# Kernel optimization log

Hardware: AMD Instinct MI355X
Metric: run time of the kernel (lower is better)

Reference implementation:

```python
import jax, jax.numpy as jnp
import numpy as np

N_NODES = 100000
N_USERS = 60000
N_MOVIES = 40000
N_EDGES = 1200000
D_IN = 64
D_EMB = 64


def setup_inputs() -> dict:
    key = jax.random.key(0)
    ks = jax.random.split(key, 6)
    x = jax.random.normal(ks[0], (N_NODES, D_IN), dtype=jnp.float32)
    edge_index = jax.random.randint(ks[1], (2, N_EDGES), 0, N_NODES, dtype=jnp.int64)
    # Glorot-ish init for the two GCNConv linear weights
    W1 = jax.random.normal(ks[2], (D_IN, D_EMB), dtype=jnp.float32) * (1.0 / np.sqrt(D_IN))
    b1 = jnp.zeros((D_EMB,), dtype=jnp.float32)
    W2 = jax.random.normal(ks[3], (D_EMB, D_EMB), dtype=jnp.float32) * (1.0 / np.sqrt(D_EMB))
    b2 = jnp.zeros((D_EMB,), dtype=jnp.float32)
    return {"x": x, "edge_index": edge_index, "W1": W1, "b1": b1, "W2": W2, "b2": b2}


def gcn_conv(x, W, b, src, dst):
    """PyG GCNConv: D^{-1/2}(A+I)D^{-1/2} X W + b with symmetric norm and self-loops."""
    h = x @ W  # [N, D_out]
    ones = jnp.ones(src.shape[0], dtype=h.dtype)
    # degree includes self-loop (+1)
    deg = jax.ops.segment_sum(ones, dst, num_segments=N_NODES) + 1.0
    dinv = jax.lax.rsqrt(deg)  # [N]
    coef = dinv[src] * dinv[dst]  # [E]
    agg = jax.ops.segment_sum(h[src] * coef[:, None], dst, num_segments=N_NODES)
    # self-loop contribution: norm = dinv[i]^2
    return agg + h * (dinv * dinv)[:, None] + b


def reference(x, edge_index, W1, b1, W2, b2):
    src, dst = edge_index[0], edge_index[1]
    h = gcn_conv(x, W1, b1, src, dst)
    h = jax.nn.relu(h)  # dropout is identity in eval mode
    h = gcn_conv(h, W2, b2, src, dst)
    user = h[:N_USERS]
    movie = h[N_USERS:N_USERS + N_MOVIES]
    return user, movie, h
```

## Files before the change

### kernel.cpp

```cpp
#include <hip/hip_runtime.h>

#define NN 100000
#define NE 1200000
#define DD 64
#define NPART 8
#define PSZ (NN / NPART)
#define EPB 4096
#define NCHUNK ((NE + EPB - 1) / EPB)
#define SCH 1024
#define SNB ((NN + SCH - 1) / SCH)

#define KCH3 96
#define CEH3 (NE / KCH3)
#define P3 2
#define BINS3 (NN / P3)
#define BINW3 (BINS3 / 4)
#define KSEG 4
#define KPS (KCH3 / KSEG)
#define NW4 (NN / 4)

static __device__ __forceinline__ unsigned short f2bf(float f) {
    unsigned int u = __float_as_uint(f);
    u += 0x7fffu + ((u >> 16) & 1u);
    return (unsigned short)(u >> 16);
}
static __device__ __forceinline__ float bf_lo(unsigned int u) {
    return __uint_as_float(u << 16);
}
static __device__ __forceinline__ float bf_hi(unsigned int u) {
    return __uint_as_float(u & 0xffff0000u);
}

__global__ __launch_bounds__(1024) void k_hist3(const int* __restrict__ dst,
                                                unsigned char* __restrict__ H,
                                                unsigned char* __restrict__ rank8) {
    __shared__ unsigned int bins[BINW3];
    int k = blockIdx.x >> 1;
    int p = blockIdx.x & 1;
    int t = threadIdx.x;
    for (int i = t; i < BINW3; i += 1024) bins[i] = 0u;
    __syncthreads();
    int lo = p * BINS3;
    int beg = k * CEH3;
    for (int e4 = beg + t * 4; e4 < beg + CEH3; e4 += 4096) {
        int4 d4 = *(const int4*)&dst[e4];
        int dd[4] = {d4.x, d4.y, d4.z, d4.w};
#pragma unroll
        for (int j = 0; j < 4; ++j) {
            unsigned int r = (unsigned int)(dd[j] - lo);
            if (r < (unsigned int)BINS3) {
                unsigned int sh = (r & 3u) << 3;
                unsigned int old = atomicAdd(&bins[r >> 2], 1u << sh);
                rank8[e4 + j] = (unsigned char)((old >> sh) & 0xffu);
            }
        }
    }
    __syncthreads();
    unsigned int* Hw = (unsigned int*)(H + (size_t)k * NN + lo);
    for (int i = t; i < BINW3; i += 1024) Hw[i] = bins[i];
}

__global__ __launch_bounds__(256) void k_cseg_sum(const unsigned int* __restrict__ H32,
                                                  unsigned int* __restrict__ aux) {
    int wd = blockIdx.x * 256 + threadIdx.x;
    int seg = blockIdx.y;
    if (wd >= NW4) return;
    unsigned int s = 0;
#pragma unroll
    for (int k = 0; k < KPS; ++k)
        s += H32[(size_t)(seg * KPS + k) * NW4 + wd];
    aux[seg * NW4 + wd] = s;
}

__global__ __launch_bounds__(256) void k_cseg_scan(unsigned int* __restrict__ H32,
                                                   const unsigned int* __restrict__ aux,
                                                   int* __restrict__ degi) {
    int wd = blockIdx.x * 256 + threadIdx.x;
    int seg = blockIdx.y;
    if (wd >= NW4) return;
    unsigned int base = 0;
    for (int i = 0; i < seg; ++i) base += aux[i * NW4 + wd];
    unsigned int s = base;
#pragma unroll
    for (int k = 0; k < KPS; ++k) {
        size_t idx = (size_t)(seg * KPS + k) * NW4 + wd;
        unsigned int v = H32[idx];
        H32[idx] = s;
        s += v;
    }
    if (seg == KSEG - 1) {
        int4 dg;
        dg.x = (int)(s & 0xffu);
        dg.y = (int)((s >> 8) & 0xffu);
        dg.z = (int)((s >> 16) & 0xffu);
        dg.w = (int)(s >> 24);
        *(int4*)&degi[4 * wd] = dg;
    }
}

__global__ __launch_bounds__(256) void k_fill3(const int* __restrict__ src,
                                               const int* __restrict__ dst,
                                               const unsigned char* __restrict__ rank8,
                                               const unsigned char* __restrict__ H,
                                               const int* __restrict__ rowptr,
                                               int* __restrict__ csr) {
    int e4 = (blockIdx.x * 256 + threadIdx.x) * 4;
    if (e4 >= NE) return;
    int4 d4 = *(const int4*)&dst[e4];
    int4 s4 = *(const int4*)&src[e4];
    unsigned int r4 = *(const unsigned int*)&rank8[e4];
    int dd[4] = {d4.x, d4.y, d4.z, d4.w};
    int ss[4] = {s4.x, s4.y, s4.z, s4.w};
    int k = e4 / CEH3;
#pragma unroll
    for (int j = 0; j < 4; ++j) {
        int d = dd[j];
        int base = rowptr[d] + (int)H[(size_t)k * NN + d];
        csr[base + (int)((r4 >> (8 * j)) & 0xffu)] = ss[j];
    }
}

__global__ void k_hist_rank(const int* __restrict__ dst, int* __restrict__ degi,
                            int* __restrict__ rank, int ne) {
    int i = blockIdx.x * blockDim.x + threadIdx.x;
    if (i < ne) rank[i] = atomicAdd(&degi[dst[i]], 1);
}

__global__ __launch_bounds__(256) void k_hist(const int* __restrict__ dst,
                                              int* __restrict__ degi, int ne) {
    int part = blockIdx.x & (NPART - 1);
    int lo = part * PSZ, hi = lo + PSZ;
    int beg = (blockIdx.x >> 3) * EPB;
    int end = min(beg + EPB, ne);
    for (int e = beg + (int)threadIdx.x; e < end; e += 256) {
        int d = dst[e];
        if (d >= lo && d < hi) atomicAdd(&degi[d], 1);
    }
}

__global__ __launch_bounds__(256) void k_scan_local(const int* __restrict__ degi,
                                                    int* __restrict__ rowptr,
                                                    int* __restrict__ part,
                                                    float* __restrict__ dinv) {
    __shared__ int wsum[4];
    int t = threadIdx.x;
    int idx = blockIdx.x * SCH + t * 4;
    int d0 = 0, d1 = 0, d2 = 0, d3 = 0;
    if (idx + 3 < NN) {
        int4 v = *(const int4*)&degi[idx];
        d0 = v.x; d1 = v.y; d2 = v.z; d3 = v.w;
        float4 dv;
        dv.x = rsqrtf((float)d0 + 1.0f);
        dv.y = rsqrtf((float)d1 + 1.0f);
        dv.z = rsqrtf((float)d2 + 1.0f);
        dv.w = rsqrtf((float)d3 + 1.0f);
        *(float4*)&dinv[idx] = dv;
    } else {
        if (idx     < NN) { d0 = degi[idx];     dinv[idx]     = rsqrtf((float)d0 + 1.0f); }
        if (idx + 1 < NN) { d1 = degi[idx + 1]; dinv[idx + 1] = rsqrtf((float)d1 + 1.0f); }
        if (idx + 2 < NN) { d2 = degi[idx + 2]; dinv[idx + 2] = rsqrtf((float)d2 + 1.0f); }
        if (idx + 3 < NN) { d3 = degi[idx + 3]; dinv[idx + 3] = rsqrtf((float)d3 + 1.0f); }
    }
    int s = d0 + d1 + d2 + d3;
    int lane = t & 63;
    int incl = s;
#pragma unroll
    for (int off = 1; off < 64; off <<= 1) {
        int v = __shfl_up(incl, off);
        if (lane >= off) incl += v;
    }
    int wv = t >> 6;
    if (lane == 63) wsum[wv] = incl;
    __syncthreads();
    int woff = 0;
#pragma unroll
    for (int i = 0; i < 4; ++i) if (i < wv) woff += wsum[i];
    int excl = woff + incl - s;
    if (idx     < NN) rowptr[idx]     = excl;
    if (idx + 1 < NN) rowptr[idx + 1] = excl + d0;
    if (idx + 2 < NN) rowptr[idx + 2] = excl + d0 + d1;
    if (idx + 3 < NN) rowptr[idx + 3] = excl + d0 + d1 + d2;
    if (t == 255) part[blockIdx.x] = woff + incl;
}

__global__ __launch_bounds__(128) void k_scan_part(int* __restrict__ part) {
    __shared__ int sm[128];
    int t = threadIdx.x;
    int v = (t < SNB) ? part[t] : 0;
    sm[t] = v;
    __syncthreads();
    for (int off = 1; off < 128; off <<= 1) {
        int add = (t >= off) ? sm[t - off] : 0;
        __syncthreads();
        sm[t] += add;
        __syncthreads();
    }
    if (t < SNB) part[t] = sm[t] - v;
}

__global__ void k_scan_add(int* __restrict__ rowptr, const int* __restrict__ part) {
    int i = blockIdx.x * blockDim.x + threadIdx.x;
    if (i < NN) rowptr[i] += part[i >> 10];
    if (i == 0) rowptr[NN] = NE;
}

__global__ void k_fill_rank(const int* __restrict__ src, const int* __restrict__ dst,
                            const int* __restrict__ rank, const int* __restrict__ rowptr,
                            int* __restrict__ csr_src, int ne) {
    int e = blockIdx.x * blockDim.x + threadIdx.x;
    if (e < ne) csr_src[rowptr[dst[e]] + rank[e]] = src[e];
}

__global__ __launch_bounds__(256) void k_fill(const int* __restrict__ src,
                                              const int* __restrict__ dst,
                                              const int* __restrict__ rowptr,
                                              int* __restrict__ cnt,
                                              int* __restrict__ csr_src, int ne) {
    int part = blockIdx.x & (NPART - 1);
    int lo = part * PSZ, hi = lo + PSZ;
    int beg = (blockIdx.x >> 3) * EPB;
    int end = min(beg + EPB, ne);
    for (int e = beg + (int)threadIdx.x; e < end; e += 256) {
        int d = dst[e];
        if (d >= lo && d < hi) {
            int pos = rowptr[d] + atomicAdd(&cnt[d], 1);
            csr_src[pos] = src[e];
        }
    }
}

__global__ __launch_bounds__(256) void k_gemm_bf(const float* __restrict__ X,
                                                 const float* __restrict__ W,
                                                 unsigned short* __restrict__ Hb,
                                                 int nrows) {
    __shared__ float4 Ws4[64][16];
    __shared__ float  Xs[64][68];
    int tid = threadIdx.x;
    const float4* W4 = (const float4*)W;
    for (int i = tid; i < 64 * 16; i += 256) Ws4[i >> 4][i & 15] = W4[i];
    int row0 = blockIdx.x * 64;
    const float4* X4 = (const float4*)X;
    for (int i = tid; i < 64 * 16; i += 256) {
        int r = i >> 4, q = i & 15;
        int row = row0 + r;
        float4 v = make_float4(0.f, 0.f, 0.f, 0.f);
        if (row < nrows) v = X4[row * 16 + q];
        *((float4*)&Xs[r][q * 4]) = v;
    }
    __syncthreads();
    int c4 = tid & 15;
    int rg = tid >> 4;
    float4 acc0 = make_float4(0.f, 0.f, 0.f, 0.f);
    float4 acc1 = acc0, acc2 = acc0, acc3 = acc0;
#pragma unroll 4
    for (int k = 0; k < 64; ++k) {
        float4 w = Ws4[k][c4];
        float x0 = Xs[rg * 4 + 0][k];
        float x1 = Xs[rg * 4 + 1][k];
        float x2 = Xs[rg * 4 + 2][k];
        float x3 = Xs[rg * 4 + 3][k];
        acc0.x += x0 * w.x; acc0.y += x0 * w.y; acc0.z += x0 * w.z; acc0.w += x0 * w.w;
        acc1.x += x1 * w.x; acc1.y += x1 * w.y; acc1.z += x1 * w.z; acc1.w += x1 * w.w;
        acc2.x += x2 * w.x; acc2.y += x2 * w.y; acc2.z += x2 * w.z; acc2.w += x2 * w.w;
        acc3.x += x3 * w.x; acc3.y += x3 * w.y; acc3.z += x3 * w.z; acc3.w += x3 * w.w;
    }
    float4 accs[4] = {acc0, acc1, acc2, acc3};
#pragma unroll
    for (int i = 0; i < 4; ++i) {
        int row = row0 + rg * 4 + i;
        if (row < nrows) {
            ushort4 o;
            o.x = f2bf(accs[i].x); o.y = f2bf(accs[i].y);
            o.z = f2bf(accs[i].z); o.w = f2bf(accs[i].w);
            *((ushort4*)&Hb[row * 64 + c4 * 4]) = o;
        }
    }
}

__global__ __launch_bounds__(256) void k_reduce(const unsigned short* __restrict__ Hb,
                                                const int* __restrict__ rowptr,
                                                const int* __restrict__ csr_src,
                                                const float* __restrict__ dinv,
                                                const float* __restrict__ b,
                                                float* __restrict__ out0,
                                                float* __restrict__ out1,
                                                int do_relu) {
    int n = blockIdx.x * 4 + (threadIdx.x >> 6);
    if (n >= NN) return;
    int lane = threadIdx.x & 63;
    int eg = lane >> 3;
    int cg = lane & 7;
    float din = dinv[n];
    uint4 us = *(const uint4*)(Hb + (size_t)n * 64 + cg * 8);
    float acc[8];
#pragma unroll
    for (int j = 0; j < 8; ++j) acc[j] = 0.f;

    int e = rowptr[n], end = rowptr[n + 1];
    int idx0 = e + eg;
    bool v0 = idx0 < end;
    int s0 = v0 ? csr_src[idx0] : 0;
    float cf0 = v0 ? dinv[s0] * din : 0.f;
    uint4 u0 = *(const uint4*)(Hb + (size_t)s0 * 64 + cg * 8);
    int idx1 = e + 8 + eg;
    bool v1 = idx1 < end;
    int s1 = v1 ? csr_src[idx1] : 0;
    float cf1 = v1 ? dinv[s1] * din : 0.f;

#pragma unroll 2
    while (e < end) {
        uint4 u1 = *(const uint4*)(Hb + (size_t)s1 * 64 + cg * 8);
        int idx2 = e + 16 + eg;
        bool v2 = idx2 < end;
        int s2 = v2 ? csr_src[idx2] : 0;
        float cf2 = v2 ? dinv[s2] * din : 0.f;
        acc[0] += bf_lo(u0.x) * cf0;  acc[1] += bf_hi(u0.x) * cf0;
        acc[2] += bf_lo(u0.y) * cf0;  acc[3] += bf_hi(u0.y) * cf0;
        acc[4] += bf_lo(u0.z) * cf0;  acc[5] += bf_hi(u0.z) * cf0;
        acc[6] += bf_lo(u0.w) * cf0;  acc[7] += bf_hi(u0.w) * cf0;
        u0 = u1; cf0 = cf1;
        s1 = s2; cf1 = cf2;
        e += 8;
    }

#pragma unroll
    for (int j = 0; j < 8; ++j) {
        acc[j] += __shfl_xor(acc[j], 8);
        acc[j] += __shfl_xor(acc[j], 16);
        acc[j] += __shfl_xor(acc[j], 32);
    }

    if (lane < 8) {
        float dd = din * din;
        float4 b0 = *(const float4*)(b + cg * 8);
        float4 b1 = *(const float4*)(b + cg * 8 + 4);
        float4 o0, o1;
        o0.x = acc[0] + bf_lo(us.x) * dd + b0.x;
        o0.y = acc[1] + bf_hi(us.x) * dd + b0.y;
        o0.z = acc[2] + bf_lo(us.y) * dd + b0.z;
        o0.w = acc[3] + bf_hi(us.y) * dd + b0.w;
        o1.x = acc[4] + bf_lo(us.z) * dd + b1.x;
        o1.y = acc[5] + bf_hi(us.z) * dd + b1.y;
        o1.z = acc[6] + bf_lo(us.w) * dd + b1.z;
        o1.w = acc[7] + bf_hi(us.w) * dd + b1.w;
        if (do_relu) {
            o0.x = fmaxf(o0.x, 0.f); o0.y = fmaxf(o0.y, 0.f);
            o0.z = fmaxf(o0.z, 0.f); o0.w = fmaxf(o0.w, 0.f);
            o1.x = fmaxf(o1.x, 0.f); o1.y = fmaxf(o1.y, 0.f);
            o1.z = fmaxf(o1.z, 0.f); o1.w = fmaxf(o1.w, 0.f);
        }
        *(float4*)(out0 + (size_t)n * 64 + cg * 8)     = o0;
        *(float4*)(out0 + (size_t)n * 64 + cg * 8 + 4) = o1;
        if (out1) {
            *(float4*)(out1 + (size_t)n * 64 + cg * 8)     = o0;
            *(float4*)(out1 + (size_t)n * 64 + cg * 8 + 4) = o1;
        }
    }
}

__global__ void k_copy4(const float4* __restrict__ in, float4* __restrict__ out, int n4) {
    int i = blockIdx.x * blockDim.x + threadIdx.x;
    if (i < n4) out[i] = in[i];
}

extern "C" void kernel_launch(void* const* d_in, const int* in_sizes, int n_in,
                              void* d_out, int out_size, void* d_ws, size_t ws_size,
                              hipStream_t stream) {
    const float* x  = (const float*)d_in[0];
    const int*   ei = (const int*)d_in[1];
    const float* W1 = (const float*)d_in[2];
    const float* b1 = (const float*)d_in[3];
    const float* W2 = (const float*)d_in[4];
    const float* b2 = (const float*)d_in[5];
    const int* src = ei;
    const int* dst = ei + NE;

    float* A = (float*)d_out;
    float* B = (float*)d_out + (size_t)NN * DD;

    char* w = (char*)d_ws;
    size_t off = 0;
    auto alloc = [&](size_t bytes) { void* p = w + off; off += (bytes + 255) & ~(size_t)255; return p; };
    float* dinv   = (float*)alloc(NN * sizeof(float));
    int*   degi   = (int*)  alloc(NN * sizeof(int));
    int*   cnt    = (int*)  alloc(NN * sizeof(int));
    int*   rowptr = (int*)  alloc((NN + 1) * sizeof(int));
    int*   part   = (int*)  alloc(512 * sizeof(int));
    int*   csr    = (int*)  alloc(NE * sizeof(int));
    size_t off_common = off;
    void* uni = alloc((size_t)NN * DD * sizeof(unsigned short));
    size_t off_uni = off;
    size_t need_rank = off_common + (((size_t)NE * sizeof(int) + 255) & ~(size_t)255);

    bool new_path  = (ws_size >= off_uni);
    bool rank_path = !new_path && (ws_size >= need_rank);

    unsigned char* Hh    = (unsigned char*)uni;
    unsigned char* rank8 = (unsigned char*)uni + (size_t)KCH3 * NN;
    int*           rank  = (int*)uni;
    unsigned short* Bb   = new_path ? (unsigned short*)uni : (unsigned short*)B;
    bool bb_in_ws = new_path;

    if (new_path) {
        k_hist3<<<KCH3 * P3, 1024, 0, stream>>>(dst, Hh, rank8);
        dim3 cgrid((NW4 + 255) / 256, KSEG);
        k_cseg_sum<<<cgrid, 256, 0, stream>>>((unsigned int*)Hh, (unsigned int*)cnt);
        k_cseg_scan<<<cgrid, 256, 0, stream>>>((unsigned int*)Hh, (const unsigned int*)cnt, degi);
        k_scan_local<<<SNB, 256, 0, stream>>>(degi, rowptr, part, dinv);
        k_scan_part<<<1, 128, 0, stream>>>(part);
        k_scan_add<<<(NN + 255) / 256, 256, 0, stream>>>(rowptr, part);
        k_fill3<<<(NE / 4 + 255) / 256, 256, 0, stream>>>(src, dst, rank8, Hh, rowptr, csr);
    } else if (rank_path) {
        hipMemsetAsync(degi, 0, NN * sizeof(int), stream);
        k_hist_rank<<<(NE + 255) / 256, 256, 0, stream>>>(dst, degi, rank, NE);
        k_scan_local<<<SNB, 256, 0, stream>>>(degi, rowptr, part, dinv);
        k_scan_part<<<1, 128, 0, stream>>>(part);
        k_scan_add<<<(NN + 255) / 256, 256, 0, stream>>>(rowptr, part);
        k_fill_rank<<<(NE + 255) / 256, 256, 0, stream>>>(src, dst, rank, rowptr, csr, NE);
    } else {
        hipMemsetAsync(degi, 0, NN * sizeof(int), stream);
        hipMemsetAsync(cnt, 0, NN * sizeof(int), stream);
        k_hist<<<NCHUNK * NPART, 256, 0, stream>>>(dst, degi, NE);
        k_scan_local<<<SNB, 256, 0, stream>>>(degi, rowptr, part, dinv);
        k_scan_part<<<1, 128, 0, stream>>>(part);
        k_scan_add<<<(NN + 255) / 256, 256, 0, stream>>>(rowptr, part);
        k_fill<<<NCHUNK * NPART, 256, 0, stream>>>(src, dst, rowptr, cnt, csr, NE);
    }

    k_gemm_bf<<<(NN + 63) / 64, 256, 0, stream>>>(x, W1, Bb, NN);
    k_reduce<<<(NN + 3) / 4, 256, 0, stream>>>(Bb, rowptr, csr, dinv, b1, A, nullptr, 1);

    k_gemm_bf<<<(NN + 63) / 64, 256, 0, stream>>>(A, W2, Bb, NN);
    if (bb_in_ws) {
        k_reduce<<<(NN + 3) / 4, 256, 0, stream>>>(Bb, rowptr, csr, dinv, b2, A, B, 0);
    } else {
        k_reduce<<<(NN + 3) / 4, 256, 0, stream>>>(Bb, rowptr, csr, dinv, b2, A, nullptr, 0);
        k_copy4<<<(NN * DD / 4 + 255) / 256, 256, 0, stream>>>((const float4*)A, (float4*)B, NN * DD / 4);
    }
}
```

Before: 263.4 us.

## Assign one node per 8 lanes in reduce and split histogram into four partitions

The aggregation kernel now maps each node to 8 lanes, each owning 8 feature columns and walking the node's edges sequentially. Previously 64 lanes split the edges 8 ways and combined partial sums with cross-lane shuffles. This removes the shuffle reduction and the idle lanes in the epilogue, and packs 32 nodes per block instead of 4. In exchange each wavefront loops to the maximum degree among its 8 nodes, so degree imbalance costs extra iterations and per-lane latency chains get longer. Separately, the histogram kernel's partition count goes from 2 to 4, shrinking its shared-memory bin array and doubling its block count, which may raise occupancy.

```diff
diff --git a/kernel.cpp b/kernel.cpp
--- a/kernel.cpp
+++ b/kernel.cpp
@@ -12,7 +12,7 @@
 
 #define KCH3 96
 #define CEH3 (NE / KCH3)
-#define P3 2
+#define P3 4
 #define BINS3 (NN / P3)
 #define BINW3 (BINS3 / 4)
 #define KSEG 4
@@ -35,8 +35,8 @@
                                                 unsigned char* __restrict__ H,
                                                 unsigned char* __restrict__ rank8) {
     __shared__ unsigned int bins[BINW3];
-    int k = blockIdx.x >> 1;
-    int p = blockIdx.x & 1;
+    int k = blockIdx.x >> 2;
+    int p = blockIdx.x & 3;
     int t = threadIdx.x;
     for (int i = t; i < BINW3; i += 1024) bins[i] = 0u;
     __syncthreads();
@@ -285,34 +285,35 @@
                                                 float* __restrict__ out0,
                                                 float* __restrict__ out1,
                                                 int do_relu) {
-    int n = blockIdx.x * 4 + (threadIdx.x >> 6);
+    int n = blockIdx.x * 32 + (threadIdx.x >> 3);
     if (n >= NN) return;
-    int lane = threadIdx.x & 63;
-    int eg = lane >> 3;
-    int cg = lane & 7;
+    int cg = threadIdx.x & 7;
     float din = dinv[n];
     uint4 us = *(const uint4*)(Hb + (size_t)n * 64 + cg * 8);
+
+    int e0 = rowptr[n];
+    int deg = rowptr[n + 1] - e0;
+    int dmax = deg;
+    dmax = max(dmax, __shfl_xor(dmax, 8));
+    dmax = max(dmax, __shfl_xor(dmax, 16));
+    dmax = max(dmax, __shfl_xor(dmax, 32));
+
     float acc[8];
 #pragma unroll
     for (int j = 0; j < 8; ++j) acc[j] = 0.f;
 
-    int e = rowptr[n], end = rowptr[n + 1];
-    int idx0 = e + eg;
-    bool v0 = idx0 < end;
-    int s0 = v0 ? csr_src[idx0] : 0;
+    bool v0 = 0 < deg;
+    int s0 = v0 ? csr_src[e0] : 0;
     float cf0 = v0 ? dinv[s0] * din : 0.f;
     uint4 u0 = *(const uint4*)(Hb + (size_t)s0 * 64 + cg * 8);
-    int idx1 = e + 8 + eg;
-    bool v1 = idx1 < end;
-    int s1 = v1 ? csr_src[idx1] : 0;
+    bool v1 = 1 < deg;
+    int s1 = v1 ? csr_src[e0 + 1] : 0;
     float cf1 = v1 ? dinv[s1] * din : 0.f;
 
-#pragma unroll 2
-    while (e < end) {
+    for (int t = 0; t < dmax; ++t) {
         uint4 u1 = *(const uint4*)(Hb + (size_t)s1 * 64 + cg * 8);
-        int idx2 = e + 16 + eg;
-        bool v2 = idx2 < end;
-        int s2 = v2 ? csr_src[idx2] : 0;
+        bool v2 = (t + 2) < deg;
+        int s2 = v2 ? csr_src[e0 + t + 2] : 0;
         float cf2 = v2 ? dinv[s2] * din : 0.f;
         acc[0] += bf_lo(u0.x) * cf0;  acc[1] += bf_hi(u0.x) * cf0;
         acc[2] += bf_lo(u0.y) * cf0;  acc[3] += bf_hi(u0.y) * cf0;
@@ -320,41 +321,31 @@
         acc[6] += bf_lo(u0.w) * cf0;  acc[7] += bf_hi(u0.w) * cf0;
         u0 = u1; cf0 = cf1;
         s1 = s2; cf1 = cf2;
-        e += 8;
-    }
-
-#pragma unroll
-    for (int j = 0; j < 8; ++j) {
-        acc[j] += __shfl_xor(acc[j], 8);
-        acc[j] += __shfl_xor(acc[j], 16);
-        acc[j] += __shfl_xor(acc[j], 32);
-    }
-
-    if (lane < 8) {
-        float dd = din * din;
-        float4 b0 = *(const float4*)(b + cg * 8);
-        float4 b1 = *(const float4*)(b + cg * 8 + 4);
-        float4 o0, o1;
-        o0.x = acc[0] + bf_lo(us.x) * dd + b0.x;
-        o0.y = acc[1] + bf_hi(us.x) * dd + b0.y;
-        o0.z = acc[2] + bf_lo(us.y) * dd + b0.z;
-        o0.w = acc[3] + bf_hi(us.y) * dd + b0.w;
-        o1.x = acc[4] + bf_lo(us.z) * dd + b1.x;
-        o1.y = acc[5] + bf_hi(us.z) * dd + b1.y;
-        o1.z = acc[6] + bf_lo(us.w) * dd + b1.z;
-        o1.w = acc[7] + bf_hi(us.w) * dd + b1.w;
-        if (do_relu) {
-            o0.x = fmaxf(o0.x, 0.f); o0.y = fmaxf(o0.y, 0.f);
-            o0.z = fmaxf(o0.z, 0.f); o0.w = fmaxf(o0.w, 0.f);
-            o1.x = fmaxf(o1.x, 0.f); o1.y = fmaxf(o1.y, 0.f);
-            o1.z = fmaxf(o1.z, 0.f); o1.w = fmaxf(o1.w, 0.f);
-        }
-        *(float4*)(out0 + (size_t)n * 64 + cg * 8)     = o0;
-        *(float4*)(out0 + (size_t)n * 64 + cg * 8 + 4) = o1;
-        if (out1) {
-            *(float4*)(out1 + (size_t)n * 64 + cg * 8)     = o0;
-            *(float4*)(out1 + (size_t)n * 64 + cg * 8 + 4) = o1;
-        }
+    }
+
+    float dd = din * din;
+    float4 b0 = *(const float4*)(b + cg * 8);
+    float4 b1 = *(const float4*)(b + cg * 8 + 4);
+    float4 o0, o1;
+    o0.x = acc[0] + bf_lo(us.x) * dd + b0.x;
+    o0.y = acc[1] + bf_hi(us.x) * dd + b0.y;
+    o0.z = acc[2] + bf_lo(us.y) * dd + b0.z;
+    o0.w = acc[3] + bf_hi(us.y) * dd + b0.w;
+    o1.x = acc[4] + bf_lo(us.z) * dd + b1.x;
+    o1.y = acc[5] + bf_hi(us.z) * dd + b1.y;
+    o1.z = acc[6] + bf_lo(us.w) * dd + b1.z;
+    o1.w = acc[7] + bf_hi(us.w) * dd + b1.w;
+    if (do_relu) {
+        o0.x = fmaxf(o0.x, 0.f); o0.y = fmaxf(o0.y, 0.f);
+        o0.z = fmaxf(o0.z, 0.f); o0.w = fmaxf(o0.w, 0.f);
+        o1.x = fmaxf(o1.x, 0.f); o1.y = fmaxf(o1.y, 0.f);
+        o1.z = fmaxf(o1.z, 0.f); o1.w = fmaxf(o1.w, 0.f);
+    }
+    *(float4*)(out0 + (size_t)n * 64 + cg * 8)     = o0;
+    *(float4*)(out0 + (size_t)n * 64 + cg * 8 + 4) = o1;
+    if (out1) {
+        *(float4*)(out1 + (size_t)n * 64 + cg * 8)     = o0;
+        *(float4*)(out1 + (size_t)n * 64 + cg * 8 + 4) = o1;
     }
 }
 
@@ -428,13 +419,13 @@
     }
 
     k_gemm_bf<<<(NN + 63) / 64, 256, 0, stream>>>(x, W1, Bb, NN);
-    k_reduce<<<(NN + 3) / 4, 256, 0, stream>>>(Bb, rowptr, csr, dinv, b1, A, nullptr, 1);
+    k_reduce<<<(NN + 31) / 32, 256, 0, stream>>>(Bb, rowptr, csr, dinv, b1, A, nullptr, 1);
 
     k_gemm_bf<<<(NN + 63) / 64, 256, 0, stream>>>(A, W2, Bb, NN);
     if (bb_in_ws) {
-        k_reduce<<<(NN + 3) / 4, 256, 0, stream>>>(Bb, rowptr, csr, dinv, b2, A, B, 0);
+        k_reduce<<<(NN + 31) / 32, 256, 0, stream>>>(Bb, rowptr, csr, dinv, b2, A, B, 0);
     } else {
-        k_reduce<<<(NN + 3) / 4, 256, 0, stream>>>(Bb, rowptr, csr, dinv, b2, A, nullptr, 0);
+        k_reduce<<<(NN + 31) / 32, 256, 0, stream>>>(Bb, rowptr, csr, dinv, b2, A, nullptr, 0);
         k_copy4<<<(NN * DD / 4 + 255) / 256, 256, 0, stream>>>((const float4*)A, (float4*)B, NN * DD / 4);
     }
 }
```

Measured after the change: 245.2 us. 1.07x faster.
